# Performance work log

Hardware: AMD Instinct MI355X
Metric: run time of the kernel (lower is better)

The kernel has to match this reference:

```python
import jax, jax.numpy as jnp
import numpy as np

GROUPS = 32
EPS = 1e-5   # nn.GroupNorm default


def group_norm(x, gamma, beta):
    # x: [B, C, H, W]
    b, c, h, w = x.shape
    xg = x.reshape(b, GROUPS, c // GROUPS, h, w)
    mu = jnp.mean(xg, axis=(2, 3, 4), keepdims=True)
    var = jnp.var(xg, axis=(2, 3, 4), keepdims=True)
    xn = ((xg - mu) * jax.lax.rsqrt(var + EPS)).reshape(b, c, h, w)
    return xn * gamma[None, :, None, None] + beta[None, :, None, None]


def conv1x1(x, w, b):
    # x: [B, C, H, W], w: [O, C], b: [O]
    return jnp.einsum('bchw,oc->bohw', x, w) + b[None, :, None, None]


def setup_inputs() -> dict:
    key = jax.random.key(0)
    ks = jax.random.split(key, 10)
    B, C, H, W = 8, 512, 64, 64
    std = 1.0 / np.sqrt(C)
    inp = {
        'x': jax.random.normal(ks[0], (B, C, H, W), dtype=jnp.float32),
        'gn_gamma': jnp.ones((C,), dtype=jnp.float32),
        'gn_beta': jnp.zeros((C,), dtype=jnp.float32),
        'wq': jax.random.normal(ks[1], (C, C), dtype=jnp.float32) * std,
        'bq': jnp.zeros((C,), dtype=jnp.float32),
        'wk': jax.random.normal(ks[2], (C, C), dtype=jnp.float32) * std,
        'bk': jnp.zeros((C,), dtype=jnp.float32),
        'wv': jax.random.normal(ks[3], (C, C), dtype=jnp.float32) * std,
        'bv': jnp.zeros((C,), dtype=jnp.float32),
        'wp': jax.random.normal(ks[4], (C, C), dtype=jnp.float32) * std,
        'bp': jnp.zeros((C,), dtype=jnp.float32),
    }
    return inp


def reference(x, gn_gamma, gn_beta, wq, bq, wk, bk, wv, bv, wp, bp):
    b, c, hh, ww = x.shape
    n = hh * ww
    h = group_norm(x, gn_gamma, gn_beta)
    q = conv1x1(h, wq, bq).reshape(b, c, n).transpose(0, 2, 1)  # [B, N, C]
    k = conv1x1(h, wk, bk).reshape(b, c, n)                     # [B, C, N]
    v = conv1x1(h, wv, bv).reshape(b, c, n).transpose(0, 2, 1)  # [B, N, C]
    scale = 1.0 / jnp.sqrt(jnp.asarray(c, dtype=x.dtype))
    attn = jax.nn.softmax(jnp.einsum('bnc,bcm->bnm', q, k) * scale, axis=-1)
    out = jnp.einsum('bnm,bmc->bnc', attn, v)                   # [B, N, C]
    out = out.transpose(0, 2, 1).reshape(b, c, hh, ww)
    return x + conv1x1(out, wp, bp)
```

## Files before the change

### kernel.cpp

```cpp
#include <hip/hip_runtime.h>


typedef __attribute__((ext_vector_type(8))) __bf16 bf16x8;
typedef __attribute__((ext_vector_type(4))) float f32x4;
typedef unsigned int u32;

#define DEVICE __device__ __forceinline__

DEVICE void async_copy16(const void* g, void* l) {
  __builtin_amdgcn_global_load_lds(
      (__attribute__((address_space(1))) u32*)(g),
      (__attribute__((address_space(3))) u32*)(l),
      16, 0, 0);
}

__global__ __launch_bounds__(256) void cvt_w(
    const float* __restrict__ w0, const float* __restrict__ w1,
    const float* __restrict__ w2, const float* __restrict__ w3,
    __bf16* __restrict__ o0, __bf16* __restrict__ o1,
    __bf16* __restrict__ o2, __bf16* __restrict__ o3) {
  int idx = blockIdx.x * 256 + threadIdx.x;
  int off = idx * 8;
  int m = off >> 18;
  int r = off & 262143;
  const float* src = m == 0 ? w0 : m == 1 ? w1 : m == 2 ? w2 : w3;
  __bf16* dst = m == 0 ? o0 : m == 1 ? o1 : m == 2 ? o2 : o3;
  float4 a = *(const float4*)(src + r);
  float4 b = *(const float4*)(src + r + 4);
  bf16x8 v = {(__bf16)a.x, (__bf16)a.y, (__bf16)a.z, (__bf16)a.w,
              (__bf16)b.x, (__bf16)b.y, (__bf16)b.z, (__bf16)b.w};
  *(bf16x8*)(dst + r) = v;
}

__global__ __launch_bounds__(256) void gn_stats(const float* __restrict__ x,
                                                float* __restrict__ stats4) {
  int bg = blockIdx.x, qn = blockIdx.y;
  int t = threadIdx.x, lane = t & 63, w = t >> 6;
  float s = 0.f, ss = 0.f;
  for (int it = 0; it < 16; ++it) {
    int idx = it * 256 + t;
    int ch = idx >> 8, f4 = idx & 255;
    float4 v = *(const float4*)(x + (size_t)bg * 65536 + (size_t)ch * 4096 +
                                qn * 1024 + f4 * 4);
    s += v.x + v.y + v.z + v.w;
    ss += v.x * v.x + v.y * v.y + v.z * v.z + v.w * v.w;
  }
#pragma unroll
  for (int off = 32; off; off >>= 1) {
    s += __shfl_xor(s, off);
    ss += __shfl_xor(ss, off);
  }
  __shared__ float rs_[4], rss_[4];
  if (lane == 0) { rs_[w] = s; rss_[w] = ss; }
  __syncthreads();
  if (t == 0) {
    stats4[(bg * 4 + qn) * 2] = rs_[0] + rs_[1] + rs_[2] + rs_[3];
    stats4[(bg * 4 + qn) * 2 + 1] = rss_[0] + rss_[1] + rss_[2] + rss_[3];
  }
}

__global__ __launch_bounds__(256) void gn_apply(
    const float* __restrict__ x, const float* __restrict__ gamma,
    const float* __restrict__ beta, const float* __restrict__ stats4,
    __bf16* __restrict__ h) {
  int b = blockIdx.z, g4 = blockIdx.y;
  int n = blockIdx.x * 256 + threadIdx.x;
  float mean[4], rstd[4];
#pragma unroll
  for (int k = 0; k < 4; ++k) {
    int bg = b * 32 + g4 * 4 + k;
    float s = 0.f, ss = 0.f;
#pragma unroll
    for (int q = 0; q < 4; ++q) {
      s += stats4[(bg * 4 + q) * 2];
      ss += stats4[(bg * 4 + q) * 2 + 1];
    }
    float m = s * (1.0f / 65536.0f);
    mean[k] = m;
    rstd[k] = rsqrtf(ss * (1.0f / 65536.0f) - m * m + 1e-5f);
  }
  const float* px = x + ((size_t)b * 512 + g4 * 64) * 4096 + n;
  __bf16* dst = h + ((size_t)b * 4096 + n) * 512 + g4 * 64;
#pragma unroll
  for (int j4 = 0; j4 < 8; ++j4) {
    bf16x8 o;
#pragma unroll
    for (int e = 0; e < 8; ++e) {
      int c = j4 * 8 + e;
      int g = c >> 4;
      float v = px[(size_t)c * 4096];
      o[e] = (__bf16)((v - mean[g]) * rstd[g] * gamma[g4 * 64 + c] +
                      beta[g4 * 64 + c]);
    }
    *(bf16x8*)(dst + j4 * 8) = o;
  }
}


#define G256_PHASE(BUF, QR, QC, RDA, RDB, STAGE_STMT, TAIL_STMT)               \
  do {                                                                         \
    if (RDA) {                                                                 \
      _Pragma("unroll") for (int fr = 0; fr < 4; ++fr) {                       \
        a[fr][0] = ldA(BUF, (QR)*4 + fr, 0);                                   \
        a[fr][1] = ldA(BUF, (QR)*4 + fr, 1);                                   \
      }                                                                        \
    }                                                                          \
    if (RDB) {                                                                 \
      _Pragma("unroll") for (int fc = 0; fc < 2; ++fc) {                       \
        b[(QC)*2 + fc][0] = ldB(BUF, (QC)*2 + fc, 0);                          \
        b[(QC)*2 + fc][1] = ldB(BUF, (QC)*2 + fc, 1);                          \
      }                                                                        \
    }                                                                          \
    STAGE_STMT;                                                                \
    __builtin_amdgcn_s_barrier();                                              \
    asm volatile("s_waitcnt lgkmcnt(0)" ::: "memory");                         \
    __builtin_amdgcn_sched_barrier(0);                                         \
    __builtin_amdgcn_s_setprio(1);                                             \
    _Pragma("unroll") for (int fr = 0; fr < 4; ++fr)                           \
      _Pragma("unroll") for (int fc = 0; fc < 2; ++fc) {                       \
        acc[(QR)*4 + fr][(QC)*2 + fc] =                                        \
            __builtin_amdgcn_mfma_f32_16x16x32_bf16(                           \
                a[fr][0], b[(QC)*2 + fc][0], acc[(QR)*4 + fr][(QC)*2 + fc],    \
                0, 0, 0);                                                      \
        acc[(QR)*4 + fr][(QC)*2 + fc] =                                        \
            __builtin_amdgcn_mfma_f32_16x16x32_bf16(                           \
                a[fr][1], b[(QC)*2 + fc][1], acc[(QR)*4 + fr][(QC)*2 + fc],    \
                0, 0, 0);                                                      \
      }                                                                        \
    __builtin_amdgcn_s_setprio(0);                                             \
    TAIL_STMT;                                                                 \
    __builtin_amdgcn_sched_barrier(0);                                         \
    __builtin_amdgcn_s_barrier();                                              \
  } while (0)

#define G256_ITER(T0, T1, LAST)                                                \
  G256_PHASE(0, 0, 0, 1, 1, stage(1, 0, 0, (T1)), ((void)0));                  \
  G256_PHASE(0, 0, 1, 0, 1, stage(1, 0, 1, (T1)), ((void)0));                  \
  G256_PHASE(0, 1, 0, 1, 0,                                                    \
             if (!(LAST)) stage(0, 1, 0, (T0) + 2), ((void)0));                \
  G256_PHASE(0, 1, 1, 0, 0,                                                    \
             if (!(LAST)) stage(0, 1, 1, (T0) + 2),                            \
             if (LAST) {                                                       \
               asm volatile("s_waitcnt vmcnt(0)" ::: "memory");                \
             } else {                                                          \
               asm volatile("s_waitcnt vmcnt(4)" ::: "memory");                \
             });                                                               \
  G256_PHASE(1, 0, 0, 1, 1,                                                    \
             if (!(LAST)) stage(0, 0, 0, (T0) + 2), ((void)0));                \
  G256_PHASE(1, 0, 1, 0, 1,                                                    \
             if (!(LAST)) stage(0, 0, 1, (T0) + 2), ((void)0));                \
  G256_PHASE(1, 1, 0, 1, 0,                                                    \
             if (!(LAST)) stage(1, 1, 0, (T1) + 2), ((void)0));                \
  G256_PHASE(1, 1, 1, 0, 0,                                                    \
             if (!(LAST)) stage(1, 1, 1, (T1) + 2),                            \
             if (!(LAST)) {                                                    \
               asm volatile("s_waitcnt vmcnt(4)" ::: "memory");                \
             })

template <int EPI>
__global__ __launch_bounds__(512, 2) void gemm256(
    const __bf16* __restrict__ A, const __bf16* __restrict__ B,
    void* __restrict__ CoutV, int lda, int ldb, int ldc, int nIter, int nTM,
    int nTN, int KS, int sup8, long sA, long sKA, long sB, long sKB, long sC,
    const float* __restrict__ bias0, const float* __restrict__ bias1,
    const float* __restrict__ resid) {
  __shared__ __bf16 lds_raw[2][2][2][128][64];

  int nwg = gridDim.x, bid = blockIdx.x;
  int qq = nwg >> 3, rr = nwg & 7;
  int xcd = bid & 7, ii = bid >> 3;
  int swz = (xcd < rr ? xcd * (qq + 1) : rr * (qq + 1) + (xcd - rr) * qq) + ii;
  int tilesPerZ = nTM * nTN;
  int r = swz % tilesPerZ;
  int zz = swz / tilesPerZ;
  int tm, tn;
  if (sup8) {
    int sup = r >> 6, local = r & 63;
    int supCols = nTN >> 3;
    tm = (sup / supCols) * 8 + (local >> 3);
    tn = (sup % supCols) * 8 + (local & 7);
  } else {
    tn = r % nTN;
    tm = r / nTN;
  }
  int z = zz / KS, ks = zz % KS;
  A += (size_t)z * sA + (size_t)ks * sKA;
  B += (size_t)z * sB + (size_t)ks * sKB;
  __bf16* Cout = (__bf16*)CoutV + (size_t)zz * sC;
  int row0 = tm * 256, col0 = tn * 256;

  int tid = threadIdx.x;
  int wid = tid >> 6, lane = tid & 63;
  int wr = wid >> 2, wc = wid & 3;
  int l15 = lane & 15, l4 = lane >> 4;

  auto stage = [&](int buf, int mat, int half, int kt) {
    const __bf16* src = mat ? B : A;
    int ld = mat ? ldb : lda;
    int rbase = (mat ? col0 : row0) + half * 128;
    char* ldsbase = (char*)lds_raw + (((buf * 2 + mat) * 2 + half) * 16384);
#pragma unroll
    for (int L = 0; L < 2; ++L) {
      int ci = L * 512 + tid;
      int rr2 = ci >> 3, cslot = ci & 7;
      int csrc = cslot ^ (rr2 & 7);
      async_copy16(src + (size_t)(rbase + rr2) * ld + kt * 64 + csrc * 8,
                   ldsbase + (L * 512 + wid * 64) * 16);
    }
  };
  auto ldA = [&](int buf, int fr, int kh) -> bf16x8 {
    int row = fr * 16 + l15;
    int g = kh * 4 + l4;
    char* base = (char*)lds_raw + (((buf * 2 + 0) * 2 + wr) * 16384);
    return *(const bf16x8*)(base + row * 128 + ((g ^ (row & 7)) * 16));
  };
  auto ldB = [&](int buf, int fc, int kh) -> bf16x8 {
    int row = (wc & 1) * 64 + fc * 16 + l15;
    int g = kh * 4 + l4;
    char* base = (char*)lds_raw + (((buf * 2 + 1) * 2 + (wc >> 1)) * 16384);
    return *(const bf16x8*)(base + row * 128 + ((g ^ (row & 7)) * 16));
  };

  f32x4 acc[8][4] = {};
  bf16x8 a[4][2], b[4][2];

  stage(0, 1, 0, 0);
  stage(0, 1, 1, 0);
  stage(0, 0, 0, 0);
  stage(0, 0, 1, 0);
  stage(1, 1, 0, 1);
  stage(1, 1, 1, 1);
  asm volatile("s_waitcnt vmcnt(4)" ::: "memory");
  __builtin_amdgcn_sched_barrier(0);
  __builtin_amdgcn_s_barrier();

  int it = 0;
  for (; it < nIter - 1; ++it) {
    G256_ITER(2 * it, 2 * it + 1, 0);
  }
  G256_ITER(2 * it, 2 * it + 1, 1);

  int rb = row0 + wr * 128, cb = col0 + wc * 64;
  if constexpr (EPI == 3) {
#pragma unroll
    for (int fc = 0; fc < 4; ++fc) {
      int col = cb + fc * 16 + l15;
      float bb = bias0[col];
#pragma unroll
      for (int fr = 0; fr < 8; ++fr) {
        int r0 = rb + fr * 16 + l4 * 4;
        size_t idx = ((size_t)(r0 >> 12) * 512 + col) * 4096 + (r0 & 4095);
        float4 rv = *(const float4*)(resid + idx);
        float4 ov = {acc[fr][fc][0] + bb + rv.x, acc[fr][fc][1] + bb + rv.y,
                     acc[fr][fc][2] + bb + rv.z, acc[fr][fc][3] + bb + rv.w};
        *(float4*)((float*)CoutV + idx) = ov;
      }
    }
  } else {
#pragma unroll
    for (int fr = 0; fr < 8; ++fr) {
#pragma unroll
      for (int rg = 0; rg < 4; ++rg) {
        int row = rb + fr * 16 + l4 * 4 + rg;
#pragma unroll
        for (int fc = 0; fc < 4; ++fc) {
          int col = cb + fc * 16 + l15;
          float v = acc[fr][fc][rg];
          if constexpr (EPI == 1) v += col < 512 ? bias0[col] : bias1[col - 512];
          if constexpr (EPI == 2) v += bias0[row];
          Cout[(size_t)row * ldc + col] = (__bf16)v;
        }
      }
    }
  }
}

__global__ __launch_bounds__(256) void softmax_rows_bf16(__bf16* __restrict__ S) {
  int row = blockIdx.x;
  __bf16* p = S + (size_t)row * 4096;
  int t = threadIdx.x, lane = t & 63, w = t >> 6;
  const float c1 = 0.04419417382415922f * 1.4426950408889634f;
  bf16x8 v0 = *(const bf16x8*)(p + t * 16);
  bf16x8 v1 = *(const bf16x8*)(p + t * 16 + 8);
  float f[16];
  float mx = -3.4e38f;
#pragma unroll
  for (int i = 0; i < 8; ++i) { f[i] = (float)v0[i]; mx = fmaxf(mx, f[i]); }
#pragma unroll
  for (int i = 0; i < 8; ++i) { f[8 + i] = (float)v1[i]; mx = fmaxf(mx, f[8 + i]); }
#pragma unroll
  for (int off = 32; off; off >>= 1) mx = fmaxf(mx, __shfl_xor(mx, off));
  __shared__ float rm[4], rsum[4];
  if (lane == 0) rm[w] = mx;
  __syncthreads();
  float m = fmaxf(fmaxf(rm[0], rm[1]), fmaxf(rm[2], rm[3]));
  float s = 0.f;
#pragma unroll
  for (int i = 0; i < 16; ++i) {
    f[i] = exp2f((f[i] - m) * c1);
    s += f[i];
  }
#pragma unroll
  for (int off = 32; off; off >>= 1) s += __shfl_xor(s, off);
  if (lane == 0) rsum[w] = s;
  __syncthreads();
  float inv = 1.0f / (rsum[0] + rsum[1] + rsum[2] + rsum[3]);
  bf16x8 o0, o1;
#pragma unroll
  for (int i = 0; i < 8; ++i) o0[i] = (__bf16)(f[i] * inv);
#pragma unroll
  for (int i = 0; i < 8; ++i) o1[i] = (__bf16)(f[8 + i] * inv);
  *(bf16x8*)(p + t * 16) = o0;
  *(bf16x8*)(p + t * 16 + 8) = o1;
}

__global__ __launch_bounds__(256) void reduce4(const __bf16* __restrict__ part,
                                               __bf16* __restrict__ out) {
  int z = blockIdx.y;
  size_t e = ((size_t)blockIdx.x * 256 + threadIdx.x) * 8;
  const __bf16* p = part + (size_t)z * 4 * 2097152 + e;
  bf16x8 v0 = *(const bf16x8*)(p);
  bf16x8 v1 = *(const bf16x8*)(p + 2097152);
  bf16x8 v2 = *(const bf16x8*)(p + 2 * 2097152);
  bf16x8 v3 = *(const bf16x8*)(p + 3 * 2097152);
  bf16x8 o;
#pragma unroll
  for (int j = 0; j < 8; ++j)
    o[j] = (__bf16)((float)v0[j] + (float)v1[j] + (float)v2[j] + (float)v3[j]);
  *(bf16x8*)(out + (size_t)z * 2097152 + e) = o;
}

extern "C" void kernel_launch(void* const* d_in, const int* in_sizes, int n_in,
                              void* d_out, int out_size, void* d_ws, size_t ws_size,
                              hipStream_t stream) {
  const float* x = (const float*)d_in[0];
  const float* gamma = (const float*)d_in[1];
  const float* beta = (const float*)d_in[2];
  const float* wq = (const float*)d_in[3];
  const float* bq = (const float*)d_in[4];
  const float* wk = (const float*)d_in[5];
  const float* bk = (const float*)d_in[6];
  const float* wv = (const float*)d_in[7];
  const float* bv = (const float*)d_in[8];
  const float* wp = (const float*)d_in[9];
  const float* bp = (const float*)d_in[10];

  char* p = (char*)d_ws;
  auto alloc = [&](size_t bytes) {
    char* r = p;
    p += (bytes + 255) & ~(size_t)255;
    return r;
  };
  float* stats4 = (float*)alloc(256 * 4 * 2 * 4);
  __bf16* wqkb = (__bf16*)alloc((size_t)1024 * 512 * 2);
  __bf16* wvb = (__bf16*)alloc(512 * 512 * 2);
  __bf16* wpb = (__bf16*)alloc(512 * 512 * 2);
  __bf16* ho = (__bf16*)alloc((size_t)8 * 4096 * 512 * 2);
  __bf16* qk = (__bf16*)alloc((size_t)8 * 4096 * 1024 * 2);
  __bf16* vt = (__bf16*)alloc((size_t)8 * 512 * 4096 * 2);

  const size_t SB = (size_t)4096 * 4096 * 2;
  const size_t PB = (size_t)4 * 4096 * 512 * 2;
  size_t used = (size_t)(p - (char*)d_ws);
  size_t freeb = (ws_size > used) ? ws_size - used : 0;
  int nb = (int)(freeb / (SB + PB));
  if (nb > 8) nb = 8;
  if (nb < 1) nb = 1;
  __bf16* s = (__bf16*)alloc(SB * nb);
  __bf16* pvp = (__bf16*)alloc(PB * nb);

  cvt_w<<<512, 256, 0, stream>>>(wq, wk, wv, wp, wqkb, wqkb + 262144, wvb, wpb);
  gn_stats<<<dim3(256, 4), 256, 0, stream>>>(x, stats4);
  gn_apply<<<dim3(16, 8, 8), 256, 0, stream>>>(x, gamma, beta, stats4, ho);

  gemm256<1><<<dim3(512), 512, 0, stream>>>(
      ho, wqkb, qk, 512, 512, 1024, 4, 128, 4, 1, 0, 0, 0, 0, 0, 0,
      bq, bk, nullptr);
  gemm256<2><<<dim3(256), 512, 0, stream>>>(
      wvb, ho, vt, 512, 512, 4096, 4, 2, 16, 1, 0, 0, 0, 2097152, 0, 2097152,
      bv, nullptr, nullptr);

  __bf16* o = ho;
  for (int b0 = 0; b0 < 8; b0 += nb) {
    int zb = (8 - b0 < nb) ? (8 - b0) : nb;
    gemm256<0><<<dim3(zb * 256), 512, 0, stream>>>(
        qk + (size_t)b0 * 4194304, qk + (size_t)b0 * 4194304 + 512, s, 1024,
        1024, 4096, 4, 16, 16, 1, 1, 4194304, 0, 4194304, 0, 16777216,
        nullptr, nullptr, nullptr);
    softmax_rows_bf16<<<zb * 4096, 256, 0, stream>>>(s);
    gemm256<0><<<dim3(zb * 128), 512, 0, stream>>>(
        s, vt + (size_t)b0 * 2097152, pvp, 4096, 4096, 512, 8, 16, 2, 4, 0,
        16777216, 1024, 2097152, 1024, 2097152, nullptr, nullptr, nullptr);
    reduce4<<<dim3(1024, zb), 256, 0, stream>>>(pvp, o + (size_t)b0 * 2097152);
  }
  gemm256<3><<<dim3(256), 512, 0, stream>>>(
      o, wpb, d_out, 512, 512, 0, 4, 128, 2, 1, 0, 0, 0, 0, 0, 0,
      bp, nullptr, x);
}
```

Before: 581.0 us.

## Fuse softmax exponent and normalization into the PV GEMM operand load

```diff
diff --git a/kernel.cpp b/kernel.cpp
--- a/kernel.cpp
+++ b/kernel.cpp
@@ -13,6 +13,8 @@
       (__attribute__((address_space(3))) u32*)(l),
       16, 0, 0);
 }
+
+#define C1_SM 0.06376979862047992f
 
 __global__ __launch_bounds__(256) void cvt_w(
     const float* __restrict__ w0, const float* __restrict__ w1,
@@ -163,7 +165,7 @@
     void* __restrict__ CoutV, int lda, int ldb, int ldc, int nIter, int nTM,
     int nTN, int KS, int sup8, long sA, long sKA, long sB, long sKB, long sC,
     const float* __restrict__ bias0, const float* __restrict__ bias1,
-    const float* __restrict__ resid) {
+    const float* __restrict__ resid, const float2* __restrict__ rstat) {
   __shared__ __bf16 lds_raw[2][2][2][128][64];
 
   int nwg = gridDim.x, bid = blockIdx.x;
@@ -194,6 +196,15 @@
   int wr = wid >> 2, wc = wid & 3;
   int l15 = lane & 15, l4 = lane >> 4;
 
+  const float2* rsz = nullptr;
+  float mc1r[8];
+  if constexpr (EPI == 4) {
+    rsz = rstat + (size_t)z * 4096;
+#pragma unroll
+    for (int f = 0; f < 8; ++f)
+      mc1r[f] = rsz[row0 + wr * 128 + f * 16 + l15].x;
+  }
+
   auto stage = [&](int buf, int mat, int half, int kt) {
     const __bf16* src = mat ? B : A;
     int ld = mat ? ldb : lda;
@@ -212,7 +223,15 @@
     int row = fr * 16 + l15;
     int g = kh * 4 + l4;
     char* base = (char*)lds_raw + (((buf * 2 + 0) * 2 + wr) * 16384);
-    return *(const bf16x8*)(base + row * 128 + ((g ^ (row & 7)) * 16));
+    bf16x8 v = *(const bf16x8*)(base + row * 128 + ((g ^ (row & 7)) * 16));
+    if constexpr (EPI == 4) {
+      bf16x8 e;
+#pragma unroll
+      for (int j = 0; j < 8; ++j)
+        e[j] = (__bf16)exp2f((float)v[j] * C1_SM - mc1r[fr]);
+      return e;
+    }
+    return v;
   };
   auto ldB = [&](int buf, int fc, int kh) -> bf16x8 {
     int row = (wc & 1) * 64 + fc * 16 + l15;
@@ -262,12 +281,15 @@
 #pragma unroll
       for (int rg = 0; rg < 4; ++rg) {
         int row = rb + fr * 16 + l4 * 4 + rg;
+        float rscale = 1.f;
+        if constexpr (EPI == 4) rscale = rsz[row].y;
 #pragma unroll
         for (int fc = 0; fc < 4; ++fc) {
           int col = cb + fc * 16 + l15;
           float v = acc[fr][fc][rg];
           if constexpr (EPI == 1) v += col < 512 ? bias0[col] : bias1[col - 512];
           if constexpr (EPI == 2) v += bias0[row];
+          if constexpr (EPI == 4) v *= rscale;
           Cout[(size_t)row * ldc + col] = (__bf16)v;
         }
       }
@@ -275,11 +297,11 @@
   }
 }
 
-__global__ __launch_bounds__(256) void softmax_rows_bf16(__bf16* __restrict__ S) {
+__global__ __launch_bounds__(256) void softmax_stats(
+    const __bf16* __restrict__ S, float2* __restrict__ rs) {
   int row = blockIdx.x;
-  __bf16* p = S + (size_t)row * 4096;
+  const __bf16* p = S + (size_t)row * 4096;
   int t = threadIdx.x, lane = t & 63, w = t >> 6;
-  const float c1 = 0.04419417382415922f * 1.4426950408889634f;
   bf16x8 v0 = *(const bf16x8*)(p + t * 16);
   bf16x8 v1 = *(const bf16x8*)(p + t * 16 + 8);
   float f[16];
@@ -296,22 +318,15 @@
   float m = fmaxf(fmaxf(rm[0], rm[1]), fmaxf(rm[2], rm[3]));
   float s = 0.f;
 #pragma unroll
-  for (int i = 0; i < 16; ++i) {
-    f[i] = exp2f((f[i] - m) * c1);
-    s += f[i];
-  }
+  for (int i = 0; i < 16; ++i) s += exp2f((f[i] - m) * C1_SM);
 #pragma unroll
   for (int off = 32; off; off >>= 1) s += __shfl_xor(s, off);
   if (lane == 0) rsum[w] = s;
   __syncthreads();
-  float inv = 1.0f / (rsum[0] + rsum[1] + rsum[2] + rsum[3]);
-  bf16x8 o0, o1;
-#pragma unroll
-  for (int i = 0; i < 8; ++i) o0[i] = (__bf16)(f[i] * inv);
-#pragma unroll
-  for (int i = 0; i < 8; ++i) o1[i] = (__bf16)(f[8 + i] * inv);
-  *(bf16x8*)(p + t * 16) = o0;
-  *(bf16x8*)(p + t * 16 + 8) = o1;
+  if (t == 0) {
+    float total = rsum[0] + rsum[1] + rsum[2] + rsum[3];
+    rs[row] = make_float2(m * C1_SM, 1.0f / total);
+  }
 }
 
 __global__ __launch_bounds__(256) void reduce4(const __bf16* __restrict__ part,
@@ -358,6 +373,7 @@
   __bf16* ho = (__bf16*)alloc((size_t)8 * 4096 * 512 * 2);
   __bf16* qk = (__bf16*)alloc((size_t)8 * 4096 * 1024 * 2);
   __bf16* vt = (__bf16*)alloc((size_t)8 * 512 * 4096 * 2);
+  float2* rs = (float2*)alloc((size_t)8 * 4096 * sizeof(float2));
 
   const size_t SB = (size_t)4096 * 4096 * 2;
   const size_t PB = (size_t)4 * 4096 * 512 * 2;
@@ -375,10 +391,10 @@
 
   gemm256<1><<<dim3(512), 512, 0, stream>>>(
       ho, wqkb, qk, 512, 512, 1024, 4, 128, 4, 1, 0, 0, 0, 0, 0, 0,
-      bq, bk, nullptr);
+      bq, bk, nullptr, nullptr);
   gemm256<2><<<dim3(256), 512, 0, stream>>>(
       wvb, ho, vt, 512, 512, 4096, 4, 2, 16, 1, 0, 0, 0, 2097152, 0, 2097152,
-      bv, nullptr, nullptr);
+      bv, nullptr, nullptr, nullptr);
 
   __bf16* o = ho;
   for (int b0 = 0; b0 < 8; b0 += nb) {
@@ -386,14 +402,14 @@
     gemm256<0><<<dim3(zb * 256), 512, 0, stream>>>(
         qk + (size_t)b0 * 4194304, qk + (size_t)b0 * 4194304 + 512, s, 1024,
         1024, 4096, 4, 16, 16, 1, 1, 4194304, 0, 4194304, 0, 16777216,
-        nullptr, nullptr, nullptr);
-    softmax_rows_bf16<<<zb * 4096, 256, 0, stream>>>(s);
-    gemm256<0><<<dim3(zb * 128), 512, 0, stream>>>(
+        nullptr, nullptr, nullptr, nullptr);
+    softmax_stats<<<zb * 4096, 256, 0, stream>>>(s, rs);
+    gemm256<4><<<dim3(zb * 128), 512, 0, stream>>>(
         s, vt + (size_t)b0 * 2097152, pvp, 4096, 4096, 512, 8, 16, 2, 4, 0,
-        16777216, 1024, 2097152, 1024, 2097152, nullptr, nullptr, nullptr);
+        16777216, 1024, 2097152, 1024, 2097152, nullptr, nullptr, nullptr, rs);
     reduce4<<<dim3(1024, zb), 256, 0, stream>>>(pvp, o + (size_t)b0 * 2097152);
   }
   gemm256<3><<<dim3(256), 512, 0, stream>>>(
       o, wpb, d_out, 512, 512, 0, 4, 128, 2, 1, 0, 0, 0, 0, 0, 0,
-      bp, nullptr, x);
-}
+      bp, nullptr, x, nullptr);
+}
```

After: 939.5 us. 1.62x slower.
